# Kernel tuning notes

Hardware: AMD Instinct MI355X
Metric: run time of the kernel (lower is better)

## Reference

```python
import jax, jax.numpy as jnp
import numpy as np

B, T, C, H = 8, 2048, 1024, 64

def setup_inputs() -> dict:
    key = jax.random.key(0)
    k1, k2, k3, k4 = jax.random.split(key, 4)
    x = jax.random.normal(k1, (B, T, C), dtype=jnp.float32)
    sw = 1.0 / np.sqrt(C)  # Linear-like init scale
    Wq = jax.random.normal(k2, (C, H), dtype=jnp.float32) * sw
    Wk = jax.random.normal(k3, (C, H), dtype=jnp.float32) * sw
    Wv = jax.random.normal(k4, (C, H), dtype=jnp.float32) * sw
    return {"x": x, "Wq": Wq, "Wk": Wk, "Wv": Wv}

def reference(x, Wq, Wk, Wv):
    # Single-head causal self-attention (eval mode: dropout is identity).
    # Quantized GEMMs (QLinear / qmatmul) are represented by exact fp32 math.
    Bx, Tx, Cx = x.shape
    q = jnp.einsum('btc,ch->bth', x, Wq)          # [B,T,H]
    k = jnp.einsum('btc,ch->bth', x, Wk)          # [B,T,H]
    v = jnp.einsum('btc,ch->bth', x, Wv)          # [B,T,H]
    scale = k.shape[-1] ** -0.5
    wei = jnp.einsum('bth,bsh->bts', q, k) * scale  # [B,T,T]
    causal = jnp.tril(jnp.ones((Tx, Tx), dtype=bool))
    wei = jnp.where(causal, wei, -jnp.inf)
    wei = jax.nn.softmax(wei, axis=-1)
    out = jnp.einsum('bts,bsh->bth', wei, v)      # [B,T,H]
    return out
```

## Files before the change

### kernel.cpp

```cpp
#include <hip/hip_runtime.h>
#include <math.h>

#define Bz 8
#define Tz 2048
#define Cz 1024
#define Hz 64
#define BT (Bz*Tz)

typedef __attribute__((ext_vector_type(8))) short bf16x8;
typedef __attribute__((ext_vector_type(4))) float f32x4;
typedef __attribute__((ext_vector_type(4))) unsigned short us4;

#define PSTRIDE 4160

__device__ __forceinline__ unsigned short f2bf(float f) {
    union { float f; unsigned u; } v; v.f = f;
    unsigned r = v.u + 0x7fffu + ((v.u >> 16) & 1u);
    return (unsigned short)(r >> 16);
}

__device__ __forceinline__ bf16x8 pack8(const float* s) {
    bf16x8 r;
#pragma unroll
    for (int j = 0; j < 8; j++) r[j] = (short)f2bf(s[j]);
    return r;
}

__device__ __forceinline__ void gload16(const void* g, void* l) {
    __builtin_amdgcn_global_load_lds(
        (const __attribute__((address_space(1))) void*)g,
        (__attribute__((address_space(3))) void*)l, 16, 0, 0);
}

__global__ __launch_bounds__(256)
void wprep_kernel(const float* __restrict__ Wq, const float* __restrict__ Wk,
                  const float* __restrict__ Wv, unsigned short* __restrict__ Wt)
{
    __shared__ float T[64][65];
    const int mat = blockIdx.x >> 4;
    const int k0  = (blockIdx.x & 15) * 64;
    const float* W = (mat == 0) ? Wq : (mat == 1) ? Wk : Wv;
    const int t  = threadIdx.x;
    const int rr = t >> 2;
    const int c4 = (t & 3) * 16;
#pragma unroll
    for (int j = 0; j < 4; j++) {
        float4 w4 = *(const float4*)&W[(size_t)(k0 + rr) * Hz + c4 + j * 4];
        T[c4 + j*4 + 0][rr] = w4.x;
        T[c4 + j*4 + 1][rr] = w4.y;
        T[c4 + j*4 + 2][rr] = w4.z;
        T[c4 + j*4 + 3][rr] = w4.w;
    }
    __syncthreads();
    const int nn = t >> 2;
    const int ks = (t & 3) * 16;
    float tmp[16];
#pragma unroll
    for (int j = 0; j < 16; j++) tmp[j] = T[nn][ks + j];
    unsigned short* dst = &Wt[(size_t)(mat * 64 + nn) * Cz + k0 + ks];
    *(bf16x8*)dst       = pack8(tmp);
    *(bf16x8*)(dst + 8) = pack8(tmp + 8);
}

__global__ __launch_bounds__(256, 2)
void qkv_mfma_kernel(const float* __restrict__ x, const unsigned short* __restrict__ Wt,
                     unsigned short* __restrict__ qg, unsigned short* __restrict__ kg,
                     unsigned short* __restrict__ vT)
{
    __shared__ unsigned short xs[32 * 64];
    __shared__ unsigned short ws[192 * 64];

    const int t  = threadIdx.x;
    const int M0 = blockIdx.x * 32;
    const int ln = t & 15;
    const int g  = (t & 63) >> 4;
    const int g4 = g * 4;
    const int w  = t >> 6;
    const int wr = w & 1;
    const int wc = w >> 1;
    const float SCq = 0.18033688011112042f;

    f32x4 acc[6];
#pragma unroll
    for (int i = 0; i < 6; i++) acc[i] = (f32x4){0.f, 0.f, 0.f, 0.f};

    const int xrow = t >> 3;
    const int xsl  = t & 7;
    int wn[6], wsl[6];
#pragma unroll
    for (int i = 0; i < 6; i++) {
        const int c = i * 256 + t;
        wn[i] = c >> 3; wsl[i] = c & 7;
    }

    float4 xf0, xf1;
    bf16x8 wreg[6];

    auto load_chunk = [&](int k0) {
        const float* src = &x[(size_t)(M0 + xrow) * Cz + k0 + xsl * 8];
        xf0 = *(const float4*)src;
        xf1 = *(const float4*)(src + 4);
#pragma unroll
        for (int i = 0; i < 6; i++)
            wreg[i] = *(const bf16x8*)&Wt[(size_t)wn[i] * Cz + k0 + wsl[i] * 8];
    };
    auto write_chunk = [&]() {
        float tmp[8];
        tmp[0]=xf0.x; tmp[1]=xf0.y; tmp[2]=xf0.z; tmp[3]=xf0.w;
        tmp[4]=xf1.x; tmp[5]=xf1.y; tmp[6]=xf1.z; tmp[7]=xf1.w;
        *(bf16x8*)&xs[xrow*64 + (xsl ^ (xrow & 7)) * 8] = pack8(tmp);
#pragma unroll
        for (int i = 0; i < 6; i++)
            *(bf16x8*)&ws[wn[i]*64 + (wsl[i] ^ (wn[i] & 7)) * 8] = wreg[i];
    };

    load_chunk(0);
    write_chunk();
    for (int kt = 0; kt < 16; kt++) {
        __syncthreads();
        if (kt < 15) load_chunk((kt + 1) * 64);

        bf16x8 af[2];
        const int m = wr * 16 + ln;
#pragma unroll
        for (int kc = 0; kc < 2; kc++)
            af[kc] = *(const bf16x8*)&xs[m*64 + ((kc*4 + g) ^ (m & 7)) * 8];
        __builtin_amdgcn_s_setprio(1);
#pragma unroll
        for (int ct = 0; ct < 6; ct++) {
            const int nn = wc * 96 + ct * 16 + ln;
#pragma unroll
            for (int kc = 0; kc < 2; kc++) {
                bf16x8 bf = *(const bf16x8*)&ws[nn*64 + ((kc*4 + g) ^ (nn & 7)) * 8];
                acc[ct] = __builtin_amdgcn_mfma_f32_16x16x32_bf16(af[kc], bf, acc[ct], 0, 0, 0);
            }
        }
        __builtin_amdgcn_s_setprio(0);
        __syncthreads();
        if (kt < 15) write_chunk();
    }

#pragma unroll
    for (int ct = 0; ct < 6; ct++) {
        const int col0 = wc * 96 + ct * 16;
        const int mat  = col0 >> 6;
        const int cl   = (col0 & 63) + ln;
        const int m0   = M0 + wr * 16 + g4;
        if (mat == 0) {
#pragma unroll
            for (int i = 0; i < 4; i++)
                qg[(size_t)(m0 + i) * Hz + cl] = f2bf(acc[ct][i] * SCq);
        } else if (mat == 1) {
#pragma unroll
            for (int i = 0; i < 4; i++)
                kg[(size_t)(m0 + i) * Hz + cl] = f2bf(acc[ct][i]);
        } else {
            const int b = m0 >> 11, tt = m0 & 2047;
            us4 pk;
#pragma unroll
            for (int i = 0; i < 4; i++) pk[i] = f2bf(acc[ct][i]);
            *(us4*)&vT[((size_t)b * Hz + cl) * Tz + tt] = pk;
        }
    }
}

template<int S>
__global__ __launch_bounds__(256, 4)
void attn_mfma_kernel(const unsigned short* __restrict__ qg,
                      const unsigned short* __restrict__ kg,
                      const unsigned short* __restrict__ vT,
                      float* __restrict__ pbase)
{
    __shared__ unsigned short Ks [2][64 * 64];
    __shared__ unsigned short Vts[2][64 * 64];
    __shared__ unsigned short Ps [4 * 16 * 64];

    const int bid  = blockIdx.x;
    const int c    = bid % S;
    const int tmp0 = bid / S;
    const int b    = tmp0 & 7;
    const int qt   = 31 - (tmp0 >> 3);
    if (c > qt) return;
    const int q0   = qt * 64;

    const int t  = threadIdx.x;
    const int ln = t & 15;
    const int g  = (t & 63) >> 4;
    const int g4 = g * 4;
    const int w  = t >> 6;
    const int l6 = t & 63;

    const unsigned short* qb = qg + (size_t)b * Tz * Hz;
    const unsigned short* kb = kg + (size_t)b * Tz * Hz;
    const unsigned short* vb = vT + (size_t)b * Hz * Tz;

    bf16x8 qf[2];
    {
        const int qrow = q0 + w*16 + ln;
        qf[0] = *(const bf16x8*)&qb[(size_t)qrow * Hz + g*8];
        qf[1] = *(const bf16x8*)&qb[(size_t)qrow * Hz + 32 + g*8];
    }

    const int rl  = l6 >> 3;
    const int swz = ((l6 & 7) ^ rl) * 8;
    auto issue_tile = [&](int buf, int s0) {
#pragma unroll
        for (int qq = 0; qq < 2; qq++) {
            const int row = w*16 + qq*8 + rl;
            gload16(&kb[(size_t)(s0 + row) * Hz + swz],
                    &Ks[buf][(w*16 + qq*8) * 64]);
            gload16(&vb[(size_t)row * Tz + s0 + swz],
                    &Vts[buf][(w*16 + qq*8) * 64]);
        }
    };

    f32x4 accO[4];
#pragma unroll
    for (int i = 0; i < 4; i++) accO[i] = (f32x4){0.f, 0.f, 0.f, 0.f};
    float lrow[4] = {0.f, 0.f, 0.f, 0.f};

    unsigned short* Pw = &Ps[w * 1024];

    issue_tile(0, c * 64);
    __syncthreads();
    int cur = 0;

    for (int s = c; s <= qt; s += S) {
        if (s + S <= qt) issue_tile(cur ^ 1, (s + S) * 64);

        const unsigned short* Kc = &Ks[cur][0];
        const unsigned short* Vc = &Vts[cur][0];

        f32x4 accS[4];
        __builtin_amdgcn_s_setprio(1);
#pragma unroll
        for (int t4 = 0; t4 < 4; t4++) {
            accS[t4] = (f32x4){0.f, 0.f, 0.f, 0.f};
#pragma unroll
            for (int kc = 0; kc < 2; kc++) {
                const int n = t4*16 + ln;
                bf16x8 kf = *(const bf16x8*)&Kc[n*64 + ((kc*4 + g) ^ (n & 7)) * 8];
                accS[t4] = __builtin_amdgcn_mfma_f32_16x16x32_bf16(qf[kc], kf, accS[t4], 0, 0, 0);
            }
        }
        __builtin_amdgcn_s_setprio(0);

        const bool diag = (s == qt);
#pragma unroll
        for (int t4 = 0; t4 < 4; t4++) {
#pragma unroll
            for (int i = 0; i < 4; i++) {
                float sv = accS[t4][i];
                if (diag && (t4*16 + ln > w*16 + g4 + i)) sv = -1e30f;
                const float p = exp2f(sv);
                lrow[i] += p;
                const int col = t4*16 + ln;
                const int row = g4 + i;
                Pw[row*64 + ((col >> 3) ^ (row & 7)) * 8 + (col & 7)] = f2bf(p);
            }
        }

        __builtin_amdgcn_s_setprio(1);
#pragma unroll
        for (int kc = 0; kc < 2; kc++) {
            bf16x8 pa = *(const bf16x8*)&Pw[ln*64 + ((kc*4 + g) ^ (ln & 7)) * 8];
#pragma unroll
            for (int ht = 0; ht < 4; ht++) {
                const int vr2 = ht*16 + ln;
                bf16x8 vf = *(const bf16x8*)&Vc[vr2*64 + ((kc*4 + g) ^ (vr2 & 7)) * 8];
                accO[ht] = __builtin_amdgcn_mfma_f32_16x16x32_bf16(pa, vf, accO[ht], 0, 0, 0);
            }
        }
        __builtin_amdgcn_s_setprio(0);

        __syncthreads();
        cur ^= 1;
    }

#pragma unroll
    for (int i = 0; i < 4; i++) {
#pragma unroll
        for (int d = 1; d < 16; d <<= 1)
            lrow[i] += __shfl_xor(lrow[i], d);
    }
    float* Op = pbase + (size_t)((b * 32 + qt) * S + c) * PSTRIDE;
#pragma unroll
    for (int ht = 0; ht < 4; ht++)
#pragma unroll
        for (int i = 0; i < 4; i++)
            Op[(size_t)(w*16 + g4 + i) * 64 + ht*16 + ln] = accO[ht][i];
    if (ln == 0) {
#pragma unroll
        for (int i = 0; i < 4; i++)
            Op[4096 + w*16 + g4 + i] = lrow[i];
    }
}

template<int S>
__global__ __launch_bounds__(256)
void combine_kernel(const float* __restrict__ pbase, float* __restrict__ out)
{
    const int bid = blockIdx.x;
    const int b   = bid >> 5;
    const int qt  = bid & 31;
    const int t   = threadIdx.x;
    const int r   = t >> 2;
    const int cg  = t & 3;

    const int nch = (qt + 1 < S) ? (qt + 1) : S;
    const float* P0 = pbase + (size_t)(b * 32 + qt) * S * PSTRIDE;

    float denom = 0.f;
    float4 o[4];
#pragma unroll
    for (int j = 0; j < 4; j++) o[j] = make_float4(0.f, 0.f, 0.f, 0.f);
    for (int cc = 0; cc < nch; cc++) {
        const float* Pc = P0 + (size_t)cc * PSTRIDE;
        denom += Pc[4096 + r];
#pragma unroll
        for (int j = 0; j < 4; j++) {
            float4 v4 = *(const float4*)&Pc[(size_t)r * 64 + cg * 16 + j * 4];
            o[j].x += v4.x; o[j].y += v4.y; o[j].z += v4.z; o[j].w += v4.w;
        }
    }
    const float inv = 1.f / denom;
    float* ob = out + ((size_t)b * Tz + qt * 64 + r) * Hz + cg * 16;
#pragma unroll
    for (int j = 0; j < 4; j++)
        *(float4*)&ob[j * 4] = make_float4(o[j].x * inv, o[j].y * inv,
                                           o[j].z * inv, o[j].w * inv);
}

extern "C" void kernel_launch(void* const* d_in, const int* in_sizes, int n_in,
                              void* d_out, int out_size, void* d_ws, size_t ws_size,
                              hipStream_t stream) {
    const float* x  = (const float*)d_in[0];
    const float* Wq = (const float*)d_in[1];
    const float* Wk = (const float*)d_in[2];
    const float* Wv = (const float*)d_in[3];

    unsigned short* Wt = (unsigned short*)d_ws;
    unsigned short* qg = Wt + 196608;
    unsigned short* kg = qg + (size_t)BT * Hz;
    unsigned short* vT = kg + (size_t)BT * Hz;
    const size_t baseShorts = 196608 + 3 * (size_t)BT * Hz;
    float* pbase = (float*)((char*)d_ws + baseShorts * 2);
    float* out = (float*)d_out;

    wprep_kernel<<<48, 256, 0, stream>>>(Wq, Wk, Wv, Wt);
    qkv_mfma_kernel<<<BT / 32, 256, 0, stream>>>(x, Wt, qg, kg, vT);

    const size_t base = baseShorts * 2;
    const size_t per  = (size_t)8 * 32 * PSTRIDE * 4;
    if (ws_size >= base + 8 * per) {
        attn_mfma_kernel<8><<<8 * 32 * 8, 256, 0, stream>>>(qg, kg, vT, pbase);
        combine_kernel<8><<<256, 256, 0, stream>>>(pbase, out);
    } else if (ws_size >= base + 4 * per) {
        attn_mfma_kernel<4><<<8 * 32 * 4, 256, 0, stream>>>(qg, kg, vT, pbase);
        combine_kernel<4><<<256, 256, 0, stream>>>(pbase, out);
    } else {
        attn_mfma_kernel<1><<<8 * 32 * 1, 256, 0, stream>>>(qg, kg, vT, pbase);
        combine_kernel<1><<<256, 256, 0, stream>>>(pbase, out);
    }
}
```

Baseline: 52.16 us.

## Stream QKV GEMM tiles via async global-to-LDS loads with double buffering

Result: slower. 53.45 us (+2.5%).

```diff
diff --git a/kernel.cpp b/kernel.cpp
--- a/kernel.cpp
+++ b/kernel.cpp
@@ -26,6 +26,15 @@
     return r;
 }
 
+__device__ __forceinline__ bf16x8 pack8f4(float4 a, float4 b) {
+    bf16x8 r;
+    r[0] = (short)f2bf(a.x); r[1] = (short)f2bf(a.y);
+    r[2] = (short)f2bf(a.z); r[3] = (short)f2bf(a.w);
+    r[4] = (short)f2bf(b.x); r[5] = (short)f2bf(b.y);
+    r[6] = (short)f2bf(b.z); r[7] = (short)f2bf(b.w);
+    return r;
+}
+
 __device__ __forceinline__ void gload16(const void* g, void* l) {
     __builtin_amdgcn_global_load_lds(
         (const __attribute__((address_space(1))) void*)g,
@@ -34,11 +43,12 @@
 
 __global__ __launch_bounds__(256)
 void wprep_kernel(const float* __restrict__ Wq, const float* __restrict__ Wk,
-                  const float* __restrict__ Wv, unsigned short* __restrict__ Wt)
+                  const float* __restrict__ Wv, unsigned short* __restrict__ Wti)
 {
     __shared__ float T[64][65];
     const int mat = blockIdx.x >> 4;
-    const int k0  = (blockIdx.x & 15) * 64;
+    const int kt  = blockIdx.x & 15;
+    const int k0  = kt * 64;
     const float* W = (mat == 0) ? Wq : (mat == 1) ? Wk : Wv;
     const int t  = threadIdx.x;
     const int rr = t >> 2;
@@ -52,92 +62,86 @@
         T[c4 + j*4 + 3][rr] = w4.w;
     }
     __syncthreads();
-    const int nn = t >> 2;
-    const int ks = (t & 3) * 16;
+    const int nn  = t >> 2;
+    const int sl0 = (t & 3) * 2;
+    const int n   = mat * 64 + nn;
     float tmp[16];
 #pragma unroll
-    for (int j = 0; j < 16; j++) tmp[j] = T[nn][ks + j];
-    unsigned short* dst = &Wt[(size_t)(mat * 64 + nn) * Cz + k0 + ks];
-    *(bf16x8*)dst       = pack8(tmp);
-    *(bf16x8*)(dst + 8) = pack8(tmp + 8);
+    for (int j = 0; j < 16; j++) tmp[j] = T[nn][sl0 * 8 + j];
+    unsigned short* base = &Wti[(size_t)kt * 12288 + n * 64];
+    *(bf16x8*)&base[((sl0    ) ^ (n & 7)) * 8] = pack8(tmp);
+    *(bf16x8*)&base[((sl0 + 1) ^ (n & 7)) * 8] = pack8(tmp + 8);
 }
 
 __global__ __launch_bounds__(256, 2)
-void qkv_mfma_kernel(const float* __restrict__ x, const unsigned short* __restrict__ Wt,
+void qkv_mfma_kernel(const float* __restrict__ x, const unsigned short* __restrict__ Wti,
                      unsigned short* __restrict__ qg, unsigned short* __restrict__ kg,
                      unsigned short* __restrict__ vT)
 {
-    __shared__ unsigned short xs[32 * 64];
-    __shared__ unsigned short ws[192 * 64];
-
-    const int t  = threadIdx.x;
-    const int M0 = blockIdx.x * 32;
-    const int ln = t & 15;
-    const int g  = (t & 63) >> 4;
-    const int g4 = g * 4;
-    const int w  = t >> 6;
-    const int wr = w & 1;
-    const int wc = w >> 1;
+    __shared__ __align__(16) float          xsF[2][32 * 64];
+    __shared__ __align__(16) unsigned short ws [2][192 * 64];
+
+    const int t    = threadIdx.x;
+    const int M0   = blockIdx.x * 32;
+    const int ln   = t & 15;
+    const int g    = (t & 63) >> 4;
+    const int g4   = g * 4;
+    const int w    = t >> 6;
+    const int wr   = w & 1;
+    const int wc   = w >> 1;
+    const int lane = t & 63;
     const float SCq = 0.18033688011112042f;
 
     f32x4 acc[6];
 #pragma unroll
     for (int i = 0; i < 6; i++) acc[i] = (f32x4){0.f, 0.f, 0.f, 0.f};
 
-    const int xrow = t >> 3;
-    const int xsl  = t & 7;
-    int wn[6], wsl[6];
-#pragma unroll
-    for (int i = 0; i < 6; i++) {
-        const int c = i * 256 + t;
-        wn[i] = c >> 3; wsl[i] = c & 7;
-    }
-
-    float4 xf0, xf1;
-    bf16x8 wreg[6];
-
-    auto load_chunk = [&](int k0) {
-        const float* src = &x[(size_t)(M0 + xrow) * Cz + k0 + xsl * 8];
-        xf0 = *(const float4*)src;
-        xf1 = *(const float4*)(src + 4);
-#pragma unroll
-        for (int i = 0; i < 6; i++)
-            wreg[i] = *(const bf16x8*)&Wt[(size_t)wn[i] * Cz + k0 + wsl[i] * 8];
+    auto issue = [&](int buf, int kt) {
+        const int k0 = kt * 64;
+#pragma unroll
+        for (int j = 0; j < 2; j++) {
+            const int r  = w * 8 + j * 4 + (lane >> 4);
+            const int sl = (lane & 15) ^ (r & 7);
+            gload16(&x[(size_t)(M0 + r) * Cz + k0 + sl * 4],
+                    &xsF[buf][(w * 8 + j * 4) * 64]);
+        }
+#pragma unroll
+        for (int j = 0; j < 6; j++) {
+            const int jj = w * 6 + j;
+            gload16(&Wti[(size_t)kt * 12288 + jj * 512 + lane * 8],
+                    &ws[buf][jj * 512]);
+        }
     };
-    auto write_chunk = [&]() {
-        float tmp[8];
-        tmp[0]=xf0.x; tmp[1]=xf0.y; tmp[2]=xf0.z; tmp[3]=xf0.w;
-        tmp[4]=xf1.x; tmp[5]=xf1.y; tmp[6]=xf1.z; tmp[7]=xf1.w;
-        *(bf16x8*)&xs[xrow*64 + (xsl ^ (xrow & 7)) * 8] = pack8(tmp);
-#pragma unroll
-        for (int i = 0; i < 6; i++)
-            *(bf16x8*)&ws[wn[i]*64 + (wsl[i] ^ (wn[i] & 7)) * 8] = wreg[i];
-    };
-
-    load_chunk(0);
-    write_chunk();
+
+    issue(0, 0);
+    __syncthreads();
+    int cur = 0;
+
     for (int kt = 0; kt < 16; kt++) {
-        __syncthreads();
-        if (kt < 15) load_chunk((kt + 1) * 64);
+        if (kt < 15) issue(cur ^ 1, kt + 1);
 
         bf16x8 af[2];
-        const int m = wr * 16 + ln;
-#pragma unroll
-        for (int kc = 0; kc < 2; kc++)
-            af[kc] = *(const bf16x8*)&xs[m*64 + ((kc*4 + g) ^ (m & 7)) * 8];
+        const int row = wr * 16 + ln;
+#pragma unroll
+        for (int kc = 0; kc < 2; kc++) {
+            const int s0 = kc * 8 + g * 2;
+            float4 fa = *(const float4*)&xsF[cur][row * 64 + ((s0    ) ^ (row & 7)) * 4];
+            float4 fb = *(const float4*)&xsF[cur][row * 64 + ((s0 + 1) ^ (row & 7)) * 4];
+            af[kc] = pack8f4(fa, fb);
+        }
         __builtin_amdgcn_s_setprio(1);
 #pragma unroll
         for (int ct = 0; ct < 6; ct++) {
             const int nn = wc * 96 + ct * 16 + ln;
 #pragma unroll
             for (int kc = 0; kc < 2; kc++) {
-                bf16x8 bf = *(const bf16x8*)&ws[nn*64 + ((kc*4 + g) ^ (nn & 7)) * 8];
+                bf16x8 bf = *(const bf16x8*)&ws[cur][nn * 64 + ((kc*4 + g) ^ (nn & 7)) * 8];
                 acc[ct] = __builtin_amdgcn_mfma_f32_16x16x32_bf16(af[kc], bf, acc[ct], 0, 0, 0);
             }
         }
         __builtin_amdgcn_s_setprio(0);
         __syncthreads();
-        if (kt < 15) write_chunk();
+        cur ^= 1;
     }
 
 #pragma unroll
@@ -171,17 +175,17 @@
                       const unsigned short* __restrict__ vT,
                       float* __restrict__ pbase)
 {
-    __shared__ unsigned short Ks [2][64 * 64];
-    __shared__ unsigned short Vts[2][64 * 64];
-    __shared__ unsigned short Ps [4 * 16 * 64];
-
-    const int bid  = blockIdx.x;
-    const int c    = bid % S;
-    const int tmp0 = bid / S;
-    const int b    = tmp0 & 7;
-    const int qt   = 31 - (tmp0 >> 3);
+    __shared__ __align__(16) unsigned short Ks [2][64 * 64];
+    __shared__ __align__(16) unsigned short Vts[2][64 * 64];
+    __shared__ __align__(16) unsigned short Ps [4 * 16 * 64];
+
+    const int bid = blockIdx.x;
+    const int b   = bid & 7;
+    const int r0  = bid >> 3;
+    const int c   = r0 % S;
+    const int qt  = 31 - (r0 / S);
     if (c > qt) return;
-    const int q0   = qt * 64;
+    const int q0  = qt * 64;
 
     const int t  = threadIdx.x;
     const int ln = t & 15;
@@ -218,7 +222,6 @@
 #pragma unroll
     for (int i = 0; i < 4; i++) accO[i] = (f32x4){0.f, 0.f, 0.f, 0.f};
     float lrow[4] = {0.f, 0.f, 0.f, 0.f};
-
     unsigned short* Pw = &Ps[w * 1024];
 
     issue_tile(0, c * 64);
@@ -301,8 +304,8 @@
 void combine_kernel(const float* __restrict__ pbase, float* __restrict__ out)
 {
     const int bid = blockIdx.x;
-    const int b   = bid >> 5;
-    const int qt  = bid & 31;
+    const int b   = bid & 7;
+    const int qt  = 31 - (bid >> 3);
     const int t   = threadIdx.x;
     const int r   = t >> 2;
     const int cg  = t & 3;
@@ -339,16 +342,16 @@
     const float* Wk = (const float*)d_in[2];
     const float* Wv = (const float*)d_in[3];
 
-    unsigned short* Wt = (unsigned short*)d_ws;
-    unsigned short* qg = Wt + 196608;
-    unsigned short* kg = qg + (size_t)BT * Hz;
-    unsigned short* vT = kg + (size_t)BT * Hz;
+    unsigned short* Wti = (unsigned short*)d_ws;
+    unsigned short* qg  = Wti + 196608;
+    unsigned short* kg  = qg + (size_t)BT * Hz;
+    unsigned short* vT  = kg + (size_t)BT * Hz;
     const size_t baseShorts = 196608 + 3 * (size_t)BT * Hz;
     float* pbase = (float*)((char*)d_ws + baseShorts * 2);
     float* out = (float*)d_out;
 
-    wprep_kernel<<<48, 256, 0, stream>>>(Wq, Wk, Wv, Wt);
-    qkv_mfma_kernel<<<BT / 32, 256, 0, stream>>>(x, Wt, qg, kg, vT);
+    wprep_kernel<<<48, 256, 0, stream>>>(Wq, Wk, Wv, Wti);
+    qkv_mfma_kernel<<<BT / 32, 256, 0, stream>>>(x, Wti, qg, kg, vT);
 
     const size_t base = baseShorts * 2;
     const size_t per  = (size_t)8 * 32 * PSTRIDE * 4;
```
